# Optimization experiments

Hardware: AMD Instinct MI355X
Metric: run time of the kernel (lower is better)

## Reference

```python
import jax, jax.numpy as jnp
import numpy as np

P, Q, D = 16, 16, 1  # AR order, MA order, differencing order (init_kwargs)
S0 = 1048577         # raw series length -> 2**20 after d=1 differencing


def setup_inputs() -> dict:
    key = jax.random.key(0)
    k1, k2, k3 = jax.random.split(key, 3)
    series = jax.random.normal(k1, (1, S0, 1), dtype=jnp.float32)
    # nn.Linear(p,1,bias=False).weight flattened to (p,), applied to y[t-p:t] in order
    w_ar = jax.random.normal(k2, (P,), dtype=jnp.float32) * 0.1
    w_ma = jax.random.normal(k3, (Q,), dtype=jnp.float32) * 0.1
    return {"series": series, "w_ar": w_ar, "w_ma": w_ma}


def reference(series, w_ar, w_ma):
    # difference(): d-th order differencing (B=1, C=1 -> work on flat vector)
    y = series[0, :, 0]
    for _ in range(D):
        y = y[1:] - y[:-1]
    S = y.shape[0]
    m = max(P, Q)

    # AR windows: windows[t] = y[t-P:t] (zero-padded at front; only read when t > m >= P)
    ypad = jnp.concatenate([jnp.zeros((P,), y.dtype), y])
    windows = jnp.stack([ypad[k:k + S] for k in range(P)], axis=-1)  # (S, P)

    t_idx = jnp.arange(S)

    def step(e_hist, inp):
        # e_hist: last Q errors, oldest first (matches e_list[t-q:t] ordering)
        y_t, win, t = inp
        ar = jnp.dot(win, w_ar)
        ma = jnp.dot(e_hist, w_ma)
        pred = jnp.where(t > m, ar + ma, jnp.zeros((), y.dtype))
        err = y_t - pred
        e_hist = jnp.concatenate([e_hist[1:], err[None]])
        return e_hist, err

    e0 = jnp.zeros((Q,), y.dtype)
    _, errs = jax.lax.scan(step, e0, (y, windows, t_idx))
    # mse_loss: mean of squared one-step errors
    return jnp.mean(errs ** 2)
```

## Files before the change

### kernel.cpp

```cpp
#include <hip/hip_runtime.h>


#define S_TOTAL 1048576
#define CHUNK   1024
#define NBLK    (S_TOTAL / CHUNK)
#define LOOK    488
#define TILE    (CHUNK + LOOK)
#define NRUN    (TILE / 7)
#define ZPAD    256
#define STAGE_N 1536
#define BUF_N   (ZPAD + STAGE_N + 4)

__device__ __forceinline__ void square17(float (&cc)[17])
{
    float b[17];
    #pragma unroll
    for (int m = 0; m <= 16; ++m) {
        float s = 0.0f;
        #pragma unroll
        for (int i = 0; i <= 16; ++i) {
            int j = 2 * m - i;
            if (j >= 0 && j <= 16) {
                float t = cc[i] * cc[j];
                s = (i & 1) ? s - t : s + t;
            }
        }
        b[m] = s;
    }
    #pragma unroll
    for (int m = 0; m <= 16; ++m) cc[m] = b[m];
}

template <int LOG_S>
__device__ __forceinline__ void stage(const float* in, float* out,
                                      const float (&cc)[17], int tid)
{
    constexpr int S = 1 << LOG_S;
    __syncthreads();
    if (tid < NRUN) {
        const int r  = tid & (S - 1);
        const int q  = tid >> LOG_S;
        const int ob = r + 7 * S * q;
        float x[23];
        #pragma unroll
        for (int m = 0; m < 23; ++m)
            x[m] = in[ZPAD + ob + S * (m - 16)];
        #pragma unroll
        for (int i = 0; i < 7; ++i) {
            float acc = x[16 + i];
            #pragma unroll
            for (int j = 1; j <= 16; ++j) {
                float v = x[16 + i - j];
                acc = (j & 1) ? fmaf(-cc[j], v, acc)
                              : fmaf(cc[j], v, acc);
            }
            out[ZPAD + ob + S * i] = acc;
        }
    }
}

__global__ __launch_bounds__(256, 4) void k_arima(const float* __restrict__ series,
                                                  const float* __restrict__ w_ar,
                                                  const float* __restrict__ w_ma,
                                                  float* __restrict__ out)
{
    __shared__ float bufA[BUF_N];
    __shared__ float bufB[BUF_N];
    __shared__ float redLDS[4];

    const int tid   = threadIdx.x;
    const int L     = blockIdx.x * CHUNK - LOOK;
    const int gbase = L - 16;

    bufA[tid] = 0.0f;
    bufB[tid] = 0.0f;

    if (gbase >= 0 && gbase + STAGE_N <= S_TOTAL + 1) {
        const float4* gp = (const float4*)(series + gbase);
        float4* lp = (float4*)(bufA + ZPAD);
        lp[tid] = gp[tid];
        if (tid < STAGE_N / 4 - 256) lp[256 + tid] = gp[256 + tid];
    } else {
        for (int i = tid; i < STAGE_N; i += 256) {
            int g = gbase + i;
            g = min(max(g, 0), S_TOTAL);
            bufA[ZPAD + i] = series[g];
        }
    }

    float cc[17];
    cc[0] = 1.0f;
    #pragma unroll
    for (int m = 1; m <= 16; ++m) cc[m] = w_ma[16 - m];

    __syncthreads();

    if (tid < NRUN) {
        const int o0 = tid * 7;
        float s[24], y[23];
        #pragma unroll
        for (int m = 0; m < 24; ++m) s[m] = bufA[ZPAD + o0 + m];
        #pragma unroll
        for (int m = 0; m < 23; ++m) y[m] = s[m + 1] - s[m];
        #pragma unroll
        for (int i = 0; i < 7; ++i) {
            float acc = y[16 + i];
            #pragma unroll
            for (int j = 1; j <= 16; ++j)
                acc = fmaf(-w_ar[16 - j], y[16 + i - j], acc);
            if (L < 17) {
                int t = L + o0 + i;
                if (t <= 16) {
                    acc = 0.0f;
                    if (t >= 1) {
                        acc = y[16 + i];
                        for (int j = 1; j < t; ++j)
                            acc += w_ma[16 - j] * y[16 + i - j];
                    }
                }
            }
            bufB[ZPAD + o0 + i] = acc;
        }
    }

    stage<0>(bufB, bufA, cc, tid);  square17(cc);
    stage<1>(bufA, bufB, cc, tid);  square17(cc);
    stage<2>(bufB, bufA, cc, tid);  square17(cc);
    stage<3>(bufA, bufB, cc, tid);  square17(cc);

    {
        __syncthreads();
        const int r    = tid & 15;
        const int g    = tid >> 4;
        const int base = ZPAD + LOOK + ((g << 6) - 192) + r;
        float h[12];
        #pragma unroll
        for (int j = 0; j < 12; ++j) h[j] = 0.0f;
        float acc = 0.0f;
        #pragma unroll
        for (int s = 0; s < 16; ++s) {
            float e = bufB[base + (s << 4)];
            #pragma unroll
            for (int j = 0; j < 12; ++j) e = fmaf(-cc[j + 1], h[j], e);
            #pragma unroll
            for (int j = 11; j >= 1; --j) h[j] = h[j - 1];
            h[0] = e;
            if (s >= 12) acc += e * e;
        }
        #pragma unroll
        for (int off = 32; off > 0; off >>= 1)
            acc += __shfl_down(acc, off, 64);
        if ((tid & 63) == 0) redLDS[tid >> 6] = acc;
    }
    __syncthreads();
    if (tid == 0) {
        float tot = redLDS[0] + redLDS[1] + redLDS[2] + redLDS[3];
        if (blockIdx.x == 0) {
            float y0 = series[1] - series[0];
            tot += y0 * y0;
        }
        atomicAdd(out, tot * (1.0f / (float)S_TOTAL));
    }
}

extern "C" void kernel_launch(void* const* d_in, const int* in_sizes, int n_in,
                              void* d_out, int out_size, void* d_ws, size_t ws_size,
                              hipStream_t stream) {
    const float* series = (const float*)d_in[0];
    const float* w_ar   = (const float*)d_in[1];
    const float* w_ma   = (const float*)d_in[2];
    float* out = (float*)d_out;

    k_arima<<<NBLK, 256, 0, stream>>>(series, w_ar, w_ma, out);
}
```

Baseline: 75.20 us.

## Split block work into independent per-wavefront chunks with wave barriers

Each wavefront now processes its own 256-element chunk with a shorter 248-element lookback in private LDS buffers. Stage-to-stage synchronisation uses wave barriers instead of block-wide __syncthreads. One doubling stage is dropped and the final sequential recurrence runs with 16-tap history over 20 steps. This removes block-level barriers and idle threads (NRUN 216 of 256 before), at the cost of proportionally more redundant lookback work per output.

```diff
diff --git a/kernel.cpp b/kernel.cpp
--- a/kernel.cpp
+++ b/kernel.cpp
@@ -2,14 +2,16 @@
 
 
 #define S_TOTAL 1048576
-#define CHUNK   1024
-#define NBLK    (S_TOTAL / CHUNK)
-#define LOOK    488
-#define TILE    (CHUNK + LOOK)
-#define NRUN    (TILE / 7)
-#define ZPAD    256
-#define STAGE_N 1536
-#define BUF_N   (ZPAD + STAGE_N + 4)
+#define WCHUNK  256
+#define NBLK    1024
+#define WLOOK   248
+#define WTILE   504
+#define NRUNW   72
+#define SER     528
+#define GUARD   64
+#define BUFW    (GUARD + SER)
+
+__device__ __forceinline__ void wbar() { __builtin_amdgcn_wave_barrier(); }
 
 __device__ __forceinline__ void square17(float (&cc)[17])
 {
@@ -32,31 +34,34 @@
 }
 
 template <int LOG_S>
-__device__ __forceinline__ void stage(const float* in, float* out,
-                                      const float (&cc)[17], int tid)
+__device__ __forceinline__ void stageW(const float* in, float* out,
+                                       const float (&cc)[17], int lane)
 {
     constexpr int S = 1 << LOG_S;
-    __syncthreads();
-    if (tid < NRUN) {
-        const int r  = tid & (S - 1);
-        const int q  = tid >> LOG_S;
-        const int ob = r + 7 * S * q;
-        float x[23];
-        #pragma unroll
-        for (int m = 0; m < 23; ++m)
-            x[m] = in[ZPAD + ob + S * (m - 16)];
-        #pragma unroll
-        for (int i = 0; i < 7; ++i) {
-            float acc = x[16 + i];
+    wbar();
+    #pragma unroll
+    for (int r0 = 0; r0 < NRUNW; r0 += 64) {
+        const int r = r0 + lane;
+        if (r < NRUNW) {
+            const int ob = (r & (S - 1)) + 7 * S * (r >> LOG_S);
+            float x[23];
             #pragma unroll
-            for (int j = 1; j <= 16; ++j) {
-                float v = x[16 + i - j];
-                acc = (j & 1) ? fmaf(-cc[j], v, acc)
-                              : fmaf(cc[j], v, acc);
+            for (int m = 0; m < 23; ++m)
+                x[m] = in[GUARD + ob + S * (m - 16)];
+            #pragma unroll
+            for (int i = 0; i < 7; ++i) {
+                float acc = x[16 + i];
+                #pragma unroll
+                for (int j = 1; j <= 16; ++j) {
+                    float v = x[16 + i - j];
+                    acc = (j & 1) ? fmaf(-cc[j], v, acc)
+                                  : fmaf(cc[j], v, acc);
+                }
+                out[GUARD + ob + S * i] = acc;
             }
-            out[ZPAD + ob + S * i] = acc;
         }
     }
+    wbar();
 }
 
 __global__ __launch_bounds__(256, 4) void k_arima(const float* __restrict__ series,
@@ -64,27 +69,33 @@
                                                   const float* __restrict__ w_ma,
                                                   float* __restrict__ out)
 {
-    __shared__ float bufA[BUF_N];
-    __shared__ float bufB[BUF_N];
+    __shared__ __align__(16) float buf[8][BUFW];
     __shared__ float redLDS[4];
 
-    const int tid   = threadIdx.x;
-    const int L     = blockIdx.x * CHUNK - LOOK;
-    const int gbase = L - 16;
+    const int tid  = threadIdx.x;
+    const int w    = tid >> 6;
+    const int lane = tid & 63;
 
-    bufA[tid] = 0.0f;
-    bufB[tid] = 0.0f;
+    float* bufA = buf[2 * w];
+    float* bufB = buf[2 * w + 1];
 
-    if (gbase >= 0 && gbase + STAGE_N <= S_TOTAL + 1) {
+    const int wbase = (blockIdx.x * 4 + w) * WCHUNK;
+    const int T0    = wbase - WLOOK;
+    const int gbase = T0 - 16;
+
+    bufA[lane] = 0.0f;
+    bufB[lane] = 0.0f;
+
+    if (gbase >= 0 && gbase + SER <= S_TOTAL + 1) {
         const float4* gp = (const float4*)(series + gbase);
-        float4* lp = (float4*)(bufA + ZPAD);
-        lp[tid] = gp[tid];
-        if (tid < STAGE_N / 4 - 256) lp[256 + tid] = gp[256 + tid];
+        float4* lp = (float4*)(bufA + GUARD);
+        for (int p = lane; p < SER / 4; p += 64)
+            lp[p] = gp[p];
     } else {
-        for (int i = tid; i < STAGE_N; i += 256) {
+        for (int i = lane; i < SER; i += 64) {
             int g = gbase + i;
             g = min(max(g, 0), S_TOTAL);
-            bufA[ZPAD + i] = series[g];
+            bufA[GUARD + i] = series[g];
         }
     }
 
@@ -93,65 +104,68 @@
     #pragma unroll
     for (int m = 1; m <= 16; ++m) cc[m] = w_ma[16 - m];
 
-    __syncthreads();
+    wbar();
 
-    if (tid < NRUN) {
-        const int o0 = tid * 7;
-        float s[24], y[23];
-        #pragma unroll
-        for (int m = 0; m < 24; ++m) s[m] = bufA[ZPAD + o0 + m];
-        #pragma unroll
-        for (int m = 0; m < 23; ++m) y[m] = s[m + 1] - s[m];
-        #pragma unroll
-        for (int i = 0; i < 7; ++i) {
-            float acc = y[16 + i];
+    #pragma unroll
+    for (int r0 = 0; r0 < NRUNW; r0 += 64) {
+        const int r = r0 + lane;
+        if (r < NRUNW) {
+            const int o0 = 7 * r;
+            float s[24], y[23];
             #pragma unroll
-            for (int j = 1; j <= 16; ++j)
-                acc = fmaf(-w_ar[16 - j], y[16 + i - j], acc);
-            if (L < 17) {
-                int t = L + o0 + i;
-                if (t <= 16) {
-                    acc = 0.0f;
-                    if (t >= 1) {
-                        acc = y[16 + i];
-                        for (int j = 1; j < t; ++j)
-                            acc += w_ma[16 - j] * y[16 + i - j];
+            for (int m = 0; m < 24; ++m) s[m] = bufA[GUARD + o0 + m];
+            #pragma unroll
+            for (int m = 0; m < 23; ++m) y[m] = s[m + 1] - s[m];
+            #pragma unroll
+            for (int i = 0; i < 7; ++i) {
+                float acc = y[16 + i];
+                #pragma unroll
+                for (int j = 1; j <= 16; ++j)
+                    acc = fmaf(-w_ar[16 - j], y[16 + i - j], acc);
+                if (T0 < 17) {
+                    int t = T0 + o0 + i;
+                    if (t <= 16) {
+                        acc = 0.0f;
+                        if (t >= 1) {
+                            acc = y[16 + i];
+                            for (int j = 1; j < t; ++j)
+                                acc += w_ma[16 - j] * y[16 + i - j];
+                        }
                     }
                 }
+                bufB[GUARD + o0 + i] = acc;
             }
-            bufB[ZPAD + o0 + i] = acc;
         }
     }
 
-    stage<0>(bufB, bufA, cc, tid);  square17(cc);
-    stage<1>(bufA, bufB, cc, tid);  square17(cc);
-    stage<2>(bufB, bufA, cc, tid);  square17(cc);
-    stage<3>(bufA, bufB, cc, tid);  square17(cc);
+    stageW<0>(bufB, bufA, cc, lane);  square17(cc);
+    stageW<1>(bufA, bufB, cc, lane);  square17(cc);
+    stageW<2>(bufB, bufA, cc, lane);  square17(cc);
 
+    float acc = 0.0f;
     {
-        __syncthreads();
-        const int r    = tid & 15;
-        const int g    = tid >> 4;
-        const int base = ZPAD + LOOK + ((g << 6) - 192) + r;
-        float h[12];
+        const int rr   = lane & 7;
+        const int g    = lane >> 3;
+        const int base = GUARD + WLOOK + rr + 32 * g - 128;
+        float h[16];
         #pragma unroll
-        for (int j = 0; j < 12; ++j) h[j] = 0.0f;
-        float acc = 0.0f;
+        for (int j = 0; j < 16; ++j) h[j] = 0.0f;
         #pragma unroll
-        for (int s = 0; s < 16; ++s) {
-            float e = bufB[base + (s << 4)];
+        for (int s = 0; s < 20; ++s) {
+            float e = bufA[base + 8 * s];
             #pragma unroll
-            for (int j = 0; j < 12; ++j) e = fmaf(-cc[j + 1], h[j], e);
+            for (int j = 0; j < 16; ++j) e = fmaf(-cc[j + 1], h[j], e);
             #pragma unroll
-            for (int j = 11; j >= 1; --j) h[j] = h[j - 1];
+            for (int j = 15; j >= 1; --j) h[j] = h[j - 1];
             h[0] = e;
-            if (s >= 12) acc += e * e;
+            if (s >= 16) acc += e * e;
         }
-        #pragma unroll
-        for (int off = 32; off > 0; off >>= 1)
-            acc += __shfl_down(acc, off, 64);
-        if ((tid & 63) == 0) redLDS[tid >> 6] = acc;
     }
+
+    #pragma unroll
+    for (int off = 32; off > 0; off >>= 1)
+        acc += __shfl_down(acc, off, 64);
+    if (lane == 0) redLDS[w] = acc;
     __syncthreads();
     if (tid == 0) {
         float tot = redLDS[0] + redLDS[1] + redLDS[2] + redLDS[3];
```

Result: no change. 75.47 us (+0.3%).
